# Kernel tuning notes

Measured on AMD Instinct MI355X. Metric: run time of the kernel, lower is better.

The kernel has to match this reference:

```python
import jax, jax.numpy as jnp
import numpy as np

N, E, B, D = 50000, 1600000, 256, 64


def _lin(k, fan_in, fan_out):
    kw, kb = jax.random.split(k)
    bound = 1.0 / np.sqrt(fan_in)
    w = jax.random.uniform(kw, (fan_in, fan_out), jnp.float32, -bound, bound)
    b = jax.random.uniform(kb, (fan_out,), jnp.float32, -bound, bound)
    return w, b


def setup_inputs() -> dict:
    key = jax.random.key(0)
    ks = jax.random.split(key, 16)
    inp = {
        "x": jax.random.normal(ks[0], (N, D), jnp.float32),
        "edge_attr": jax.random.normal(ks[1], (E, D), jnp.float32),
        "u": jax.random.normal(ks[2], (B, D), jnp.float32),
        "edge_index": jax.random.randint(ks[3], (2, E), 0, N, jnp.int32),
        "batch": jnp.sort(jax.random.randint(ks[4], (N,), 0, B, jnp.int32)),
    }
    # three MLPs: edge (in 4D), node (in 3D), global (in 3D); dims [2D, 2D, D]
    specs = [("e", 4 * D), ("n", 3 * D), ("g", 3 * D)]
    ki = 5
    for name, in_dim in specs:
        dims = [in_dim, 2 * D, 2 * D, D]
        for li in range(3):
            w, b = _lin(ks[ki], dims[li], dims[li + 1]); ki += 1
            inp[f"{name}w{li+1}"] = w
            inp[f"{name}b{li+1}"] = b
    return inp


def _mlp(h, w1, b1, w2, b2, w3, b3):
    h = h @ w1 + b1
    h = jax.nn.relu(h) @ w2 + b2
    h = jax.nn.relu(h) @ w3 + b3
    return h


def _scatter_mean(src, idx, num_segments):
    s = jax.ops.segment_sum(src, idx, num_segments=num_segments)
    c = jax.ops.segment_sum(jnp.ones_like(src[:, :1]), idx, num_segments=num_segments)
    return s / jnp.maximum(c, 1.0)


def reference(x, edge_attr, u,
              ew1, eb1, ew2, eb2, ew3, eb3,
              nw1, nb1, nw2, nb2, nw3, nb3,
              gw1, gb1, gw2, gb2, gw3, gb3,
              edge_index, batch):
    row, col = edge_index[0], edge_index[1]
    # edge model: cat[src, dest, edge_attr, u[batch[row]]] -> MLP
    e_in = jnp.concatenate([x[row], x[col], edge_attr, u[batch[row]]], axis=1)  # [E, 4D]
    e = _mlp(e_in, ew1, eb1, ew2, eb2, ew3, eb3)  # [E, D]
    # node model: scatter_mean(edge_attr', row) cat x cat u[batch] -> MLP
    n_agg = _scatter_mean(e, row, x.shape[0])  # [N, D]
    n_in = jnp.concatenate([n_agg, x, u[batch]], axis=1)  # [N, 3D]
    xn = _mlp(n_in, nw1, nb1, nw2, nb2, nw3, nb3)  # [N, D]
    # global model: cat[u, scatter_mean(x', batch), scatter_mean(e', batch[row])]
    edge_mean = _scatter_mean(e, batch[row], u.shape[0])  # [B, D]
    node_mean = _scatter_mean(xn, batch, u.shape[0])  # [B, D]
    g_in = jnp.concatenate([u, node_mean, edge_mean], axis=1)  # [B, 3D]
    un = _mlp(g_in, gw1, gb1, gw2, gb2, gw3, gb3)  # [B, D]
    return xn, e, un
```

## Files before the change

### kernel.cpp

```cpp
#include <hip/hip_runtime.h>

#define NN 50000
#define EE 1600000
#define BBATCH 256
#define DD 64

typedef _Float16 f16;
typedef _Float16 f16x8 __attribute__((ext_vector_type(8)));
typedef float f32x4 __attribute__((ext_vector_type(4)));

#define MFMA16(a,b,c) __builtin_amdgcn_mfma_f32_16x16x32_f16((a),(b),(c),0,0,0)

constexpr int EW1_RL  = 264;
constexpr int EW1_OFF = 0;
constexpr int EW2_OFF = EW1_OFF + 128 * EW1_RL;
constexpr int EW3_OFF = EW2_OFF + 128 * 136;
constexpr int EH_OFF  = EW3_OFF + 64 * 136;
constexpr int EB_OFF  = EH_OFF + 4 * 32 * 136;
constexpr int ELDS    = EB_OFF + 640;

constexpr int NW1_RL  = 200;
constexpr int NW1_OFF = 0;
constexpr int NW2_OFF = NW1_OFF + 128 * NW1_RL;
constexpr int NW3_OFF = NW2_OFF + 128 * 136;
constexpr int NH_OFF  = NW3_OFF + 64 * 136;
constexpr int NB_OFF  = NH_OFF + 4 * 32 * 136;
constexpr int NLDS    = NB_OFF + 640;

__device__ __forceinline__ f16x8 pack8(const float* __restrict__ p) {
  f32x4 a = *(const f32x4*)p;
  f32x4 b = *(const f32x4*)(p + 4);
  f16x8 r;
  r[0]=(f16)a[0]; r[1]=(f16)a[1]; r[2]=(f16)a[2]; r[3]=(f16)a[3];
  r[4]=(f16)b[0]; r[5]=(f16)b[1]; r[6]=(f16)b[2]; r[7]=(f16)b[3];
  return r;
}
__device__ __forceinline__ f16x8 pack8s(const float* __restrict__ p, float sc) {
  f32x4 a = *(const f32x4*)p;
  f32x4 b = *(const f32x4*)(p + 4);
  a = a * sc; b = b * sc;
  f16x8 r;
  r[0]=(f16)a[0]; r[1]=(f16)a[1]; r[2]=(f16)a[2]; r[3]=(f16)a[3];
  r[4]=(f16)b[0]; r[5]=(f16)b[1]; r[6]=(f16)b[2]; r[7]=(f16)b[3];
  return r;
}
__device__ __forceinline__ f16x8 cvt8(f32x4 a, f32x4 b) {
  f16x8 r;
  r[0]=(f16)a[0]; r[1]=(f16)a[1]; r[2]=(f16)a[2]; r[3]=(f16)a[3];
  r[4]=(f16)b[0]; r[5]=(f16)b[1]; r[6]=(f16)b[2]; r[7]=(f16)b[3];
  return r;
}

template<int KSL, int W1RL, int W1O, int W2O, int W3O>
__device__ __forceinline__ void mlp3_core(f16* __restrict__ sm,
    const float* __restrict__ b1l, const float* __restrict__ b2l,
    const float* __restrict__ b3l,
    const f16x8 (&A1)[2][KSL], const int hb, const int r15, const int g,
    f32x4 (&acc3)[2][4])
{
  #pragma unroll
  for (int hh = 0; hh < 2; ++hh) {
    f32x4 acc[2][4];
    #pragma unroll
    for (int nt = 0; nt < 4; ++nt) {
      const float bv = b1l[(hh*4 + nt)*16 + r15];
      acc[0][nt] = (f32x4){bv, bv, bv, bv};
      acc[1][nt] = acc[0][nt];
    }
    #pragma unroll
    for (int s = 0; s < KSL; ++s) {
      #pragma unroll
      for (int nt = 0; nt < 4; ++nt) {
        const f16x8 bf = *(const f16x8*)&sm[W1O + ((hh*4+nt)*16 + r15) * W1RL + s*32 + g*8];
        acc[0][nt] = MFMA16(A1[0][s], bf, acc[0][nt]);
        acc[1][nt] = MFMA16(A1[1][s], bf, acc[1][nt]);
      }
    }
    #pragma unroll
    for (int mt = 0; mt < 2; ++mt)
      #pragma unroll
      for (int nt = 0; nt < 4; ++nt)
        #pragma unroll
        for (int i = 0; i < 4; ++i)
          sm[hb + (mt*16 + g*4 + i)*136 + (hh*4+nt)*16 + r15] =
              (f16)fmaxf(acc[mt][nt][i], 0.f);
  }

  f16x8 A2[2][4];
  #pragma unroll
  for (int mt = 0; mt < 2; ++mt)
    #pragma unroll
    for (int s = 0; s < 4; ++s)
      A2[mt][s] = *(const f16x8*)&sm[hb + (mt*16 + r15)*136 + s*32 + g*8];

  #pragma unroll
  for (int hh = 0; hh < 2; ++hh) {
    f32x4 acc[2][4];
    #pragma unroll
    for (int nt = 0; nt < 4; ++nt) {
      const float bv = b2l[(hh*4 + nt)*16 + r15];
      acc[0][nt] = (f32x4){bv, bv, bv, bv};
      acc[1][nt] = acc[0][nt];
    }
    #pragma unroll
    for (int s = 0; s < 4; ++s) {
      #pragma unroll
      for (int nt = 0; nt < 4; ++nt) {
        const f16x8 bf = *(const f16x8*)&sm[W2O + ((hh*4+nt)*16 + r15)*136 + s*32 + g*8];
        acc[0][nt] = MFMA16(A2[0][s], bf, acc[0][nt]);
        acc[1][nt] = MFMA16(A2[1][s], bf, acc[1][nt]);
      }
    }
    #pragma unroll
    for (int mt = 0; mt < 2; ++mt)
      #pragma unroll
      for (int nt = 0; nt < 4; ++nt)
        #pragma unroll
        for (int i = 0; i < 4; ++i)
          sm[hb + (mt*16 + g*4 + i)*136 + (hh*4+nt)*16 + r15] =
              (f16)fmaxf(acc[mt][nt][i], 0.f);
  }

  f16x8 A3[2][4];
  #pragma unroll
  for (int mt = 0; mt < 2; ++mt)
    #pragma unroll
    for (int s = 0; s < 4; ++s)
      A3[mt][s] = *(const f16x8*)&sm[hb + (mt*16 + r15)*136 + s*32 + g*8];

  #pragma unroll
  for (int nt = 0; nt < 4; ++nt) {
    const float bv = b3l[nt*16 + r15];
    acc3[0][nt] = (f32x4){bv, bv, bv, bv};
    acc3[1][nt] = acc3[0][nt];
  }
  #pragma unroll
  for (int s = 0; s < 4; ++s) {
    #pragma unroll
    for (int nt = 0; nt < 4; ++nt) {
      const f16x8 bf = *(const f16x8*)&sm[W3O + (nt*16 + r15)*136 + s*32 + g*8];
      acc3[0][nt] = MFMA16(A3[0][s], bf, acc3[0][nt]);
      acc3[1][nt] = MFMA16(A3[1][s], bf, acc3[1][nt]);
    }
  }
}

__global__ void transpose_cvt(const float* __restrict__ w, f16* __restrict__ wt,
                              int in_dim, int out_dim) {
  int tid = blockIdx.x * 256 + threadIdx.x;
  int total = in_dim * out_dim;
  if (tid < total) {
    int o = tid / in_dim, i = tid - o * in_dim;
    wt[tid] = (f16)w[(size_t)i * out_dim + o];
  }
}

__global__ void count_kernel(const int* __restrict__ ei, int* __restrict__ deg) {
  int tid = blockIdx.x * 256 + threadIdx.x;
  if (tid < EE) atomicAdd(&deg[ei[tid]], 1);
}

__global__ __launch_bounds__(1024) void scan_kernel(const int* __restrict__ deg,
                                                    int* __restrict__ offs,
                                                    int* __restrict__ cursor) {
  const int t = threadIdx.x;
  const int per = (NN + 1023) / 1024;
  const int s0 = t * per;
  int s1 = s0 + per; if (s1 > NN) s1 = NN;
  int sum = 0;
  for (int i = s0; i < s1; ++i) sum += deg[i];
  const int lane = t & 63, wid = t >> 6;
  int v = sum;
  #pragma unroll
  for (int off = 1; off < 64; off <<= 1) {
    int o = __shfl_up(v, off);
    if (lane >= off) v += o;
  }
  __shared__ int wsums[16];
  __shared__ int wexcl[16];
  if (lane == 63) wsums[wid] = v;
  __syncthreads();
  if (t == 0) { int run = 0; for (int k = 0; k < 16; ++k) { wexcl[k] = run; run += wsums[k]; } }
  __syncthreads();
  int run = wexcl[wid] + v - sum;
  for (int i = s0; i < s1; ++i) { int d = deg[i]; offs[i] = run; cursor[i] = run; run += d; }
  if (t == 1023) offs[NN] = run;
}

__global__ void fill_kernel(const int* __restrict__ ei, int* __restrict__ cursor,
                            int* __restrict__ elist) {
  int tid = blockIdx.x * 256 + threadIdx.x;
  if (tid < EE) {
    int r = ei[tid];
    int pos = atomicAdd(&cursor[r], 1);
    elist[pos] = tid;
  }
}

__global__ __launch_bounds__(256, 1) void edge_mlp_kernel(
    const float* __restrict__ x, const float* __restrict__ ea,
    const float* __restrict__ u, const int* __restrict__ ei,
    const int* __restrict__ batch,
    const f16* __restrict__ w1t, const f16* __restrict__ w2t, const f16* __restrict__ w3t,
    const float* __restrict__ b1, const float* __restrict__ b2, const float* __restrict__ b3,
    float* __restrict__ e_out)
{
  __shared__ __align__(16) f16 sm[ELDS];
  const int t = threadIdx.x;
  for (int c = t; c < 4096; c += 256) { int r = c >> 5, kc = c & 31;
    *(uint4*)&sm[EW1_OFF + r*EW1_RL + kc*8] = *(const uint4*)&w1t[r*256 + kc*8]; }
  for (int c = t; c < 2048; c += 256) { int r = c >> 4, kc = c & 15;
    *(uint4*)&sm[EW2_OFF + r*136 + kc*8] = *(const uint4*)&w2t[r*128 + kc*8]; }
  for (int c = t; c < 1024; c += 256) { int r = c >> 4, kc = c & 15;
    *(uint4*)&sm[EW3_OFF + r*136 + kc*8] = *(const uint4*)&w3t[r*128 + kc*8]; }
  float* bias = (float*)&sm[EB_OFF];
  if (t < 128) { bias[t] = b1[t]; bias[128 + t] = b2[t]; }
  if (t < 64)  { bias[256 + t] = b3[t]; }
  __syncthreads();

  const int l = t & 63, w = t >> 6;
  const int r15 = l & 15, g = l >> 4;
  const int hb = EH_OFF + w * (32 * 136);
  const float* b1l = bias;
  const float* b2l = bias + 128;
  const float* b3l = bias + 256;

  const int stride = gridDim.x;
  const int t0 = blockIdx.x;
  const int NT = EE / 128;

  int rC[2], cC[2], bC[2];
  int rN[2], cN[2], bN[2];
  f32x4 G[2][8][2];
  f16x8 A1[2][8];

  auto issueG = [&](const int (&rr)[2], const int (&cc)[2], const int (&bb)[2], int tt) {
    #pragma unroll
    for (int mt = 0; mt < 2; ++mt) {
      const float* s0p = x  + (size_t)rr[mt] * 64 + g * 8;
      const float* s1p = x  + (size_t)cc[mt] * 64 + g * 8;
      const float* s2p = ea + ((size_t)(tt * 128 + w * 32 + mt * 16 + r15)) * 64 + g * 8;
      const float* s3p = u  + (size_t)bb[mt] * 64 + g * 8;
      #pragma unroll
      for (int s = 0; s < 8; ++s) {
        const float* p = (s < 2 ? s0p : s < 4 ? s1p : s < 6 ? s2p : s3p) + (s & 1) * 32;
        G[mt][s][0] = *(const f32x4*)p;
        G[mt][s][1] = *(const f32x4*)(p + 4);
      }
    }
  };

  {
    int rr[2], cc[2], bb[2];
    #pragma unroll
    for (int mt = 0; mt < 2; ++mt) {
      const int eid = t0 * 128 + w * 32 + mt * 16 + r15;
      rr[mt] = ei[eid]; cc[mt] = ei[EE + eid];
    }
    #pragma unroll
    for (int mt = 0; mt < 2; ++mt) bb[mt] = batch[rr[mt]];
    issueG(rr, cc, bb, t0);
    int t1 = t0 + stride; if (t1 >= NT) t1 = t0;
    #pragma unroll
    for (int mt = 0; mt < 2; ++mt) {
      const int eid = t1 * 128 + w * 32 + mt * 16 + r15;
      rC[mt] = ei[eid]; cC[mt] = ei[EE + eid];
    }
    #pragma unroll
    for (int mt = 0; mt < 2; ++mt) bC[mt] = batch[rC[mt]];
  }

  for (int tile = t0; tile < NT; tile += stride) {
    #pragma unroll
    for (int mt = 0; mt < 2; ++mt)
      #pragma unroll
      for (int s = 0; s < 8; ++s)
        A1[mt][s] = cvt8(G[mt][s][0], G[mt][s][1]);

    int t2 = tile + 2 * stride; if (t2 >= NT) t2 = t0;
    #pragma unroll
    for (int mt = 0; mt < 2; ++mt) {
      const int eid = t2 * 128 + w * 32 + mt * 16 + r15;
      rN[mt] = ei[eid]; cN[mt] = ei[EE + eid];
    }
    int t1 = tile + stride; if (t1 >= NT) t1 = t0;
    issueG(rC, cC, bC, t1);

    f32x4 acc3[2][4];
    mlp3_core<8, EW1_RL, EW1_OFF, EW2_OFF, EW3_OFF>(sm, b1l, b2l, b3l, A1, hb, r15, g, acc3);

    #pragma unroll
    for (int mt = 0; mt < 2; ++mt) bN[mt] = batch[rN[mt]];

    const int base = tile * 128 + w * 32;
    #pragma unroll
    for (int mt = 0; mt < 2; ++mt)
      #pragma unroll
      for (int nt = 0; nt < 4; ++nt)
        #pragma unroll
        for (int i = 0; i < 4; ++i) {
          const int m = base + mt * 16 + g * 4 + i;
          e_out[(size_t)m * 64 + nt * 16 + r15] = acc3[mt][nt][i];
        }

    #pragma unroll
    for (int mt = 0; mt < 2; ++mt) { rC[mt] = rN[mt]; cC[mt] = cN[mt]; bC[mt] = bN[mt]; }
  }
}

__global__ void nsum_kernel(const float* __restrict__ e_src, const int* __restrict__ offs,
                            const int* __restrict__ elist, float* __restrict__ n_sum) {
  const int l = threadIdx.x & 63;
  const int wid = (blockIdx.x * blockDim.x + threadIdx.x) >> 6;
  const int nw = (gridDim.x * blockDim.x) >> 6;
  for (int node = wid; node < NN; node += nw) {
    const int s = offs[node], e = offs[node + 1];
    float acc = 0.f;
    int j = s;
    for (; j + 4 <= e; j += 4) {
      const int e0 = elist[j], e1 = elist[j+1], e2 = elist[j+2], e3 = elist[j+3];
      float v0 = e_src[(size_t)e0 * 64 + l];
      float v1 = e_src[(size_t)e1 * 64 + l];
      float v2 = e_src[(size_t)e2 * 64 + l];
      float v3 = e_src[(size_t)e3 * 64 + l];
      acc += (v0 + v1) + (v2 + v3);
    }
    for (; j < e; ++j) acc += e_src[(size_t)elist[j] * 64 + l];
    n_sum[(size_t)node * 64 + l] = acc;
  }
}

__global__ __launch_bounds__(256, 1) void node_mlp_kernel(
    const float* __restrict__ x, const float* __restrict__ u,
    const int* __restrict__ batch, const float* __restrict__ n_sum,
    const int* __restrict__ deg,
    const f16* __restrict__ w1t, const f16* __restrict__ w2t, const f16* __restrict__ w3t,
    const float* __restrict__ b1, const float* __restrict__ b2, const float* __restrict__ b3,
    float* __restrict__ xn_out)
{
  __shared__ __align__(16) f16 sm[NLDS];
  const int t = threadIdx.x;
  for (int c = t; c < 3072; c += 256) { int r = c / 24, kc = c - r * 24;
    *(uint4*)&sm[NW1_OFF + r*NW1_RL + kc*8] = *(const uint4*)&w1t[r*192 + kc*8]; }
  for (int c = t; c < 2048; c += 256) { int r = c >> 4, kc = c & 15;
    *(uint4*)&sm[NW2_OFF + r*136 + kc*8] = *(const uint4*)&w2t[r*128 + kc*8]; }
  for (int c = t; c < 1024; c += 256) { int r = c >> 4, kc = c & 15;
    *(uint4*)&sm[NW3_OFF + r*136 + kc*8] = *(const uint4*)&w3t[r*128 + kc*8]; }
  float* bias = (float*)&sm[NB_OFF];
  if (t < 128) { bias[t] = b1[t]; bias[128 + t] = b2[t]; }
  if (t < 64)  { bias[256 + t] = b3[t]; }
  __syncthreads();

  const int l = t & 63, w = t >> 6;
  const int r15 = l & 15, g = l >> 4;
  const int hb = NH_OFF + w * (32 * 136);
  const int base = blockIdx.x * 128 + w * 32;

  f16x8 A1[2][6];
  #pragma unroll
  for (int mt = 0; mt < 2; ++mt) {
    int raw = base + mt * 16 + r15;
    int node = raw < NN ? raw : NN - 1;
    float inv = 1.0f / fmaxf((float)deg[node], 1.0f);
    const float* sA = n_sum + (size_t)node * 64;
    const float* sB = x + (size_t)node * 64;
    const float* sC = u + (size_t)batch[node] * 64;
    #pragma unroll
    for (int s = 0; s < 6; ++s) {
      const int off = (s & 1) * 32 + g * 8;
      if (s < 2)      A1[mt][s] = pack8s(sA + off, inv);
      else if (s < 4) A1[mt][s] = pack8(sB + off);
      else            A1[mt][s] = pack8(sC + off);
    }
  }
  f32x4 acc3[2][4];
  mlp3_core<6, NW1_RL, NW1_OFF, NW2_OFF, NW3_OFF>(sm, bias, bias + 128, bias + 256,
                                                  A1, hb, r15, g, acc3);
  #pragma unroll
  for (int mt = 0; mt < 2; ++mt)
    #pragma unroll
    for (int nt = 0; nt < 4; ++nt)
      #pragma unroll
      for (int i = 0; i < 4; ++i) {
        const int m = base + mt * 16 + g * 4 + i;
        if (m < NN) xn_out[(size_t)m * 64 + nt * 16 + r15] = acc3[mt][nt][i];
      }
}

__global__ void bstart_kernel(const int* __restrict__ batch, int* __restrict__ bstart) {
  int tid = blockIdx.x * 256 + threadIdx.x;
  if (tid >= NN) return;
  int b = batch[tid];
  if (tid == 0) { for (int k = 0; k <= b; ++k) bstart[k] = 0; }
  else { int pb = batch[tid - 1]; for (int k = pb + 1; k <= b; ++k) bstart[k] = tid; }
  if (tid == NN - 1) { for (int k = b + 1; k <= BBATCH; ++k) bstart[k] = NN; }
}

__global__ void batch_sum_kernel(const float* __restrict__ xn, const float* __restrict__ n_sum,
                                 const int* __restrict__ deg, const int* __restrict__ bstart,
                                 float* __restrict__ nbsum, float* __restrict__ ebsum,
                                 int* __restrict__ ncnt, int* __restrict__ ecnt) {
  __shared__ float red0[256];
  __shared__ float red1[256];
  __shared__ int   redi[256];
  const int b = blockIdx.x;
  const int s = bstart[b], e = bstart[b + 1];
  const int t = threadIdx.x, c = t & 63, j0 = t >> 6;
  float xs = 0.f, ns = 0.f; int dc = 0;
  for (int j = s + j0; j < e; j += 4) {
    xs += xn[(size_t)j * 64 + c];
    ns += n_sum[(size_t)j * 64 + c];
    if (c == 0) dc += deg[j];
  }
  red0[t] = xs; red1[t] = ns; redi[t] = dc;
  __syncthreads();
  if (t < 128) { red0[t] += red0[t + 128]; red1[t] += red1[t + 128]; redi[t] += redi[t + 128]; }
  __syncthreads();
  if (t < 64) {
    float a0 = red0[t] + red0[t + 64];
    float a1 = red1[t] + red1[t + 64];
    nbsum[b * 64 + t] = a0;
    ebsum[b * 64 + t] = a1;
    if (t == 0) { ncnt[b] = e - s; ecnt[b] = redi[0] + redi[64]; }
  }
}

__global__ __launch_bounds__(256, 1) void global_mlp_kernel(
    const float* __restrict__ u, const float* __restrict__ nbsum,
    const float* __restrict__ ebsum, const int* __restrict__ ncnt,
    const int* __restrict__ ecnt,
    const f16* __restrict__ w1t, const f16* __restrict__ w2t, const f16* __restrict__ w3t,
    const float* __restrict__ b1, const float* __restrict__ b2, const float* __restrict__ b3,
    float* __restrict__ un_out)
{
  __shared__ __align__(16) f16 sm[NLDS];
  const int t = threadIdx.x;
  for (int c = t; c < 3072; c += 256) { int r = c / 24, kc = c - r * 24;
    *(uint4*)&sm[NW1_OFF + r*NW1_RL + kc*8] = *(const uint4*)&w1t[r*192 + kc*8]; }
  for (int c = t; c < 2048; c += 256) { int r = c >> 4, kc = c & 15;
    *(uint4*)&sm[NW2_OFF + r*136 + kc*8] = *(const uint4*)&w2t[r*128 + kc*8]; }
  for (int c = t; c < 1024; c += 256) { int r = c >> 4, kc = c & 15;
    *(uint4*)&sm[NW3_OFF + r*136 + kc*8] = *(const uint4*)&w3t[r*128 + kc*8]; }
  float* bias = (float*)&sm[NB_OFF];
  if (t < 128) { bias[t] = b1[t]; bias[128 + t] = b2[t]; }
  if (t < 64)  { bias[256 + t] = b3[t]; }
  __syncthreads();

  const int l = t & 63, w = t >> 6;
  const int r15 = l & 15, g = l >> 4;
  const int hb = NH_OFF + w * (32 * 136);
  const int base = blockIdx.x * 128 + w * 32;

  f16x8 A1[2][6];
  #pragma unroll
  for (int mt = 0; mt < 2; ++mt) {
    const int r = base + mt * 16 + r15;
    const float invn = 1.0f / fmaxf((float)ncnt[r], 1.0f);
    const float inve = 1.0f / fmaxf((float)ecnt[r], 1.0f);
    const float* sA = u + (size_t)r * 64;
    const float* sB = nbsum + (size_t)r * 64;
    const float* sC = ebsum + (size_t)r * 64;
    #pragma unroll
    for (int s = 0; s < 6; ++s) {
      const int off = (s & 1) * 32 + g * 8;
      if (s < 2)      A1[mt][s] = pack8(sA + off);
      else if (s < 4) A1[mt][s] = pack8s(sB + off, invn);
      else            A1[mt][s] = pack8s(sC + off, inve);
    }
  }
  f32x4 acc3[2][4];
  mlp3_core<6, NW1_RL, NW1_OFF, NW2_OFF, NW3_OFF>(sm, bias, bias + 128, bias + 256,
                                                  A1, hb, r15, g, acc3);
  #pragma unroll
  for (int mt = 0; mt < 2; ++mt)
    #pragma unroll
    for (int nt = 0; nt < 4; ++nt)
      #pragma unroll
      for (int i = 0; i < 4; ++i) {
        const int m = base + mt * 16 + g * 4 + i;
        un_out[(size_t)m * 64 + nt * 16 + r15] = acc3[mt][nt][i];
      }
}

extern "C" void kernel_launch(void* const* d_in, const int* in_sizes, int n_in,
                              void* d_out, int out_size, void* d_ws, size_t ws_size,
                              hipStream_t stream)
{
  (void)in_sizes; (void)n_in; (void)out_size; (void)ws_size;
  const float* x     = (const float*)d_in[0];
  const float* ea    = (const float*)d_in[1];
  const float* u     = (const float*)d_in[2];
  const int*   ei    = (const int*)d_in[3];
  const int*   batch = (const int*)d_in[4];
  const float* ew1 = (const float*)d_in[5];  const float* eb1 = (const float*)d_in[6];
  const float* ew2 = (const float*)d_in[7];  const float* eb2 = (const float*)d_in[8];
  const float* ew3 = (const float*)d_in[9];  const float* eb3 = (const float*)d_in[10];
  const float* nw1 = (const float*)d_in[11]; const float* nb1 = (const float*)d_in[12];
  const float* nw2 = (const float*)d_in[13]; const float* nb2 = (const float*)d_in[14];
  const float* nw3 = (const float*)d_in[15]; const float* nb3 = (const float*)d_in[16];
  const float* gw1 = (const float*)d_in[17]; const float* gb1 = (const float*)d_in[18];
  const float* gw2 = (const float*)d_in[19]; const float* gb2 = (const float*)d_in[20];
  const float* gw3 = (const float*)d_in[21]; const float* gb3 = (const float*)d_in[22];

  float* xn_out = (float*)d_out;
  float* e_out  = xn_out + (size_t)NN * DD;
  float* un_out = e_out + (size_t)EE * DD;

  char* p = (char*)d_ws;
  auto alloc = [&](size_t bytes) -> void* {
    void* r = (void*)p; p += (bytes + 255) & ~(size_t)255; return r;
  };
  f16* wtE1 = (f16*)alloc(256 * 128 * 2);
  f16* wtE2 = (f16*)alloc(128 * 128 * 2);
  f16* wtE3 = (f16*)alloc(128 * 64 * 2);
  f16* wtN1 = (f16*)alloc(192 * 128 * 2);
  f16* wtN2 = (f16*)alloc(128 * 128 * 2);
  f16* wtN3 = (f16*)alloc(128 * 64 * 2);
  f16* wtG1 = (f16*)alloc(192 * 128 * 2);
  f16* wtG2 = (f16*)alloc(128 * 128 * 2);
  f16* wtG3 = (f16*)alloc(128 * 64 * 2);
  int* deg    = (int*)alloc((size_t)NN * 4);
  int* offs   = (int*)alloc((size_t)(NN + 1) * 4);
  int* cursor = (int*)alloc((size_t)NN * 4);
  int* elist  = (int*)alloc((size_t)EE * 4);
  int* bstart = (int*)alloc((size_t)(BBATCH + 1) * 4);
  float* nbsum = (float*)alloc((size_t)BBATCH * 64 * 4);
  float* ebsum = (float*)alloc((size_t)BBATCH * 64 * 4);
  int* ncnt = (int*)alloc((size_t)BBATCH * 4);
  int* ecnt = (int*)alloc((size_t)BBATCH * 4);
  float* n_sum = (float*)alloc((size_t)NN * 64 * 4);

  transpose_cvt<<<dim3((256*128 + 255)/256), dim3(256), 0, stream>>>(ew1, wtE1, 256, 128);
  transpose_cvt<<<dim3((128*128 + 255)/256), dim3(256), 0, stream>>>(ew2, wtE2, 128, 128);
  transpose_cvt<<<dim3((128*64  + 255)/256), dim3(256), 0, stream>>>(ew3, wtE3, 128, 64);
  transpose_cvt<<<dim3((192*128 + 255)/256), dim3(256), 0, stream>>>(nw1, wtN1, 192, 128);
  transpose_cvt<<<dim3((128*128 + 255)/256), dim3(256), 0, stream>>>(nw2, wtN2, 128, 128);
  transpose_cvt<<<dim3((128*64  + 255)/256), dim3(256), 0, stream>>>(nw3, wtN3, 128, 64);
  transpose_cvt<<<dim3((192*128 + 255)/256), dim3(256), 0, stream>>>(gw1, wtG1, 192, 128);
  transpose_cvt<<<dim3((128*128 + 255)/256), dim3(256), 0, stream>>>(gw2, wtG2, 128, 128);
  transpose_cvt<<<dim3((128*64  + 255)/256), dim3(256), 0, stream>>>(gw3, wtG3, 128, 64);

  hipMemsetAsync(deg, 0, (size_t)NN * 4, stream);
  count_kernel<<<dim3(6250), dim3(256), 0, stream>>>(ei, deg);
  scan_kernel<<<dim3(1), dim3(1024), 0, stream>>>(deg, offs, cursor);
  fill_kernel<<<dim3(6250), dim3(256), 0, stream>>>(ei, cursor, elist);

  edge_mlp_kernel<<<dim3(256), dim3(256), 0, stream>>>(
      x, ea, u, ei, batch, wtE1, wtE2, wtE3, eb1, eb2, eb3, e_out);

  nsum_kernel<<<dim3(2048), dim3(256), 0, stream>>>(e_out, offs, elist, n_sum);

  node_mlp_kernel<<<dim3((NN + 127) / 128), dim3(256), 0, stream>>>(
      x, u, batch, n_sum, deg, wtN1, wtN2, wtN3, nb1, nb2, nb3, xn_out);

  bstart_kernel<<<dim3((NN + 255) / 256), dim3(256), 0, stream>>>(batch, bstart);
  batch_sum_kernel<<<dim3(BBATCH), dim3(256), 0, stream>>>(
      xn_out, n_sum, deg, bstart, nbsum, ebsum, ncnt, ecnt);

  global_mlp_kernel<<<dim3(2), dim3(256), 0, stream>>>(
      u, nbsum, ebsum, ncnt, ecnt, wtG1, wtG2, wtG3, gb1, gb2, gb3, un_out);
}
```

Before: 842.7 us.

## Widen edge MLP blocks, inline MLP with overlapped gathers, add fp16 edge copy for aggregation

```diff
diff --git a/kernel.cpp b/kernel.cpp
--- a/kernel.cpp
+++ b/kernel.cpp
@@ -16,7 +16,7 @@
 constexpr int EW2_OFF = EW1_OFF + 128 * EW1_RL;
 constexpr int EW3_OFF = EW2_OFF + 128 * 136;
 constexpr int EH_OFF  = EW3_OFF + 64 * 136;
-constexpr int EB_OFF  = EH_OFF + 4 * 32 * 136;
+constexpr int EB_OFF  = EH_OFF + 8 * 16 * 136;
 constexpr int ELDS    = EB_OFF + 640;
 
 constexpr int NW1_RL  = 200;
@@ -145,14 +145,26 @@
   }
 }
 
-__global__ void transpose_cvt(const float* __restrict__ w, f16* __restrict__ wt,
-                              int in_dim, int out_dim) {
+__global__ void transpose_all(
+    const float* __restrict__ e1, const float* __restrict__ e2, const float* __restrict__ e3,
+    const float* __restrict__ n1, const float* __restrict__ n2, const float* __restrict__ n3,
+    const float* __restrict__ q1, const float* __restrict__ q2, const float* __restrict__ q3,
+    f16* __restrict__ dst) {
   int tid = blockIdx.x * 256 + threadIdx.x;
-  int total = in_dim * out_dim;
-  if (tid < total) {
-    int o = tid / in_dim, i = tid - o * in_dim;
-    wt[tid] = (f16)w[(size_t)i * out_dim + o];
-  }
+  const int o1=32768,o2=49152,o3=57344,o4=81920,o5=98304,o6=106496,o7=131072,o8=147456,o9=155648;
+  if (tid >= o9) return;
+  const float* src; int in, od, rel;
+  if      (tid < o1) { src=e1; in=256; od=128; rel=tid;    }
+  else if (tid < o2) { src=e2; in=128; od=128; rel=tid-o1; }
+  else if (tid < o3) { src=e3; in=128; od=64;  rel=tid-o2; }
+  else if (tid < o4) { src=n1; in=192; od=128; rel=tid-o3; }
+  else if (tid < o5) { src=n2; in=128; od=128; rel=tid-o4; }
+  else if (tid < o6) { src=n3; in=128; od=64;  rel=tid-o5; }
+  else if (tid < o7) { src=q1; in=192; od=128; rel=tid-o6; }
+  else if (tid < o8) { src=q2; in=128; od=128; rel=tid-o7; }
+  else               { src=q3; in=128; od=64;  rel=tid-o8; }
+  int o = rel / in, i = rel - o * in;
+  dst[tid] = (f16)src[(size_t)i * od + o];
 }
 
 __global__ void count_kernel(const int* __restrict__ ei, int* __restrict__ deg) {
@@ -197,37 +209,33 @@
   }
 }
 
-__global__ __launch_bounds__(256, 1) void edge_mlp_kernel(
+__global__ __launch_bounds__(512, 2) void edge_mlp_kernel(
     const float* __restrict__ x, const float* __restrict__ ea,
     const float* __restrict__ u, const int* __restrict__ ei,
     const int* __restrict__ batch,
     const f16* __restrict__ w1t, const f16* __restrict__ w2t, const f16* __restrict__ w3t,
     const float* __restrict__ b1, const float* __restrict__ b2, const float* __restrict__ b3,
-    float* __restrict__ e_out)
+    float* __restrict__ e_out, f16* __restrict__ e16)
 {
   __shared__ __align__(16) f16 sm[ELDS];
   const int t = threadIdx.x;
-  for (int c = t; c < 4096; c += 256) { int r = c >> 5, kc = c & 31;
+  for (int c = t; c < 4096; c += 512) { int r = c >> 5, kc = c & 31;
     *(uint4*)&sm[EW1_OFF + r*EW1_RL + kc*8] = *(const uint4*)&w1t[r*256 + kc*8]; }
-  for (int c = t; c < 2048; c += 256) { int r = c >> 4, kc = c & 15;
+  for (int c = t; c < 2048; c += 512) { int r = c >> 4, kc = c & 15;
     *(uint4*)&sm[EW2_OFF + r*136 + kc*8] = *(const uint4*)&w2t[r*128 + kc*8]; }
-  for (int c = t; c < 1024; c += 256) { int r = c >> 4, kc = c & 15;
+  for (int c = t; c < 1024; c += 512) { int r = c >> 4, kc = c & 15;
     *(uint4*)&sm[EW3_OFF + r*136 + kc*8] = *(const uint4*)&w3t[r*128 + kc*8]; }
   float* bias = (float*)&sm[EB_OFF];
   if (t < 128) { bias[t] = b1[t]; bias[128 + t] = b2[t]; }
-  if (t < 64)  { bias[256 + t] = b3[t]; }
+  else if (t < 192) { bias[256 + (t - 128)] = b3[t - 128]; }
   __syncthreads();
 
   const int l = t & 63, w = t >> 6;
   const int r15 = l & 15, g = l >> 4;
-  const int hb = EH_OFF + w * (32 * 136);
-  const float* b1l = bias;
-  const float* b2l = bias + 128;
-  const float* b3l = bias + 256;
-
+  const int hb = EH_OFF + w * (16 * 136);
+  const int NT = EE / 256;
   const int stride = gridDim.x;
   const int t0 = blockIdx.x;
-  const int NT = EE / 128;
 
   int rC[2], cC[2], bC[2];
   int rN[2], cN[2], bN[2];
@@ -239,7 +247,7 @@
     for (int mt = 0; mt < 2; ++mt) {
       const float* s0p = x  + (size_t)rr[mt] * 64 + g * 8;
       const float* s1p = x  + (size_t)cc[mt] * 64 + g * 8;
-      const float* s2p = ea + ((size_t)(tt * 128 + w * 32 + mt * 16 + r15)) * 64 + g * 8;
+      const float* s2p = ea + ((size_t)(tt * 256 + w * 32 + mt * 16 + r15)) * 64 + g * 8;
       const float* s3p = u  + (size_t)bb[mt] * 64 + g * 8;
       #pragma unroll
       for (int s = 0; s < 8; ++s) {
@@ -254,7 +262,7 @@
     int rr[2], cc[2], bb[2];
     #pragma unroll
     for (int mt = 0; mt < 2; ++mt) {
-      const int eid = t0 * 128 + w * 32 + mt * 16 + r15;
+      const int eid = t0 * 256 + w * 32 + mt * 16 + r15;
       rr[mt] = ei[eid]; cc[mt] = ei[EE + eid];
     }
     #pragma unroll
@@ -263,36 +271,127 @@
     int t1 = t0 + stride; if (t1 >= NT) t1 = t0;
     #pragma unroll
     for (int mt = 0; mt < 2; ++mt) {
-      const int eid = t1 * 128 + w * 32 + mt * 16 + r15;
+      const int eid = t1 * 256 + w * 32 + mt * 16 + r15;
       rC[mt] = ei[eid]; cC[mt] = ei[EE + eid];
     }
     #pragma unroll
     for (int mt = 0; mt < 2; ++mt) bC[mt] = batch[rC[mt]];
-  }
-
-  for (int tile = t0; tile < NT; tile += stride) {
     #pragma unroll
     for (int mt = 0; mt < 2; ++mt)
       #pragma unroll
       for (int s = 0; s < 8; ++s)
         A1[mt][s] = cvt8(G[mt][s][0], G[mt][s][1]);
-
+  }
+
+  for (int tile = t0; tile < NT; tile += stride) {
     int t2 = tile + 2 * stride; if (t2 >= NT) t2 = t0;
     #pragma unroll
     for (int mt = 0; mt < 2; ++mt) {
-      const int eid = t2 * 128 + w * 32 + mt * 16 + r15;
+      const int eid = t2 * 256 + w * 32 + mt * 16 + r15;
       rN[mt] = ei[eid]; cN[mt] = ei[EE + eid];
     }
+
+    f32x4 acc1[2][2][4];
+    #pragma unroll
+    for (int hh = 0; hh < 2; ++hh)
+      #pragma unroll
+      for (int nt = 0; nt < 4; ++nt) {
+        const float bv = bias[hh*64 + nt*16 + r15];
+        acc1[hh][0][nt] = (f32x4){bv, bv, bv, bv};
+        acc1[hh][1][nt] = acc1[hh][0][nt];
+      }
+    #pragma unroll
+    for (int s = 0; s < 8; ++s)
+      #pragma unroll
+      for (int hh = 0; hh < 2; ++hh)
+        #pragma unroll
+        for (int nt = 0; nt < 4; ++nt) {
+          const f16x8 bf = *(const f16x8*)&sm[EW1_OFF + (hh*64 + nt*16 + r15)*EW1_RL + s*32 + g*8];
+          acc1[hh][0][nt] = MFMA16(A1[0][s], bf, acc1[hh][0][nt]);
+          acc1[hh][1][nt] = MFMA16(A1[1][s], bf, acc1[hh][1][nt]);
+        }
+
+    #pragma unroll
+    for (int mt = 0; mt < 2; ++mt) bN[mt] = batch[rN[mt]];
+
+    f16x8 A2[2][4];
+    #pragma unroll
+    for (int mt = 0; mt < 2; ++mt) {
+      #pragma unroll
+      for (int hh = 0; hh < 2; ++hh)
+        #pragma unroll
+        for (int nt = 0; nt < 4; ++nt)
+          #pragma unroll
+          for (int i = 0; i < 4; ++i)
+            sm[hb + (g*4 + i)*136 + hh*64 + nt*16 + r15] =
+                (f16)fmaxf(acc1[hh][mt][nt][i], 0.f);
+      #pragma unroll
+      for (int s = 0; s < 4; ++s)
+        A2[mt][s] = *(const f16x8*)&sm[hb + r15*136 + s*32 + g*8];
+    }
+
     int t1 = tile + stride; if (t1 >= NT) t1 = t0;
     issueG(rC, cC, bC, t1);
 
+    f32x4 acc2[2][2][4];
+    #pragma unroll
+    for (int hh = 0; hh < 2; ++hh)
+      #pragma unroll
+      for (int nt = 0; nt < 4; ++nt) {
+        const float bv = bias[128 + hh*64 + nt*16 + r15];
+        acc2[hh][0][nt] = (f32x4){bv, bv, bv, bv};
+        acc2[hh][1][nt] = acc2[hh][0][nt];
+      }
+    #pragma unroll
+    for (int s = 0; s < 4; ++s)
+      #pragma unroll
+      for (int hh = 0; hh < 2; ++hh)
+        #pragma unroll
+        for (int nt = 0; nt < 4; ++nt) {
+          const f16x8 bf = *(const f16x8*)&sm[EW2_OFF + (hh*64 + nt*16 + r15)*136 + s*32 + g*8];
+          acc2[hh][0][nt] = MFMA16(A2[0][s], bf, acc2[hh][0][nt]);
+          acc2[hh][1][nt] = MFMA16(A2[1][s], bf, acc2[hh][1][nt]);
+        }
+
+    f16x8 A3[2][4];
+    #pragma unroll
+    for (int mt = 0; mt < 2; ++mt) {
+      #pragma unroll
+      for (int hh = 0; hh < 2; ++hh)
+        #pragma unroll
+        for (int nt = 0; nt < 4; ++nt)
+          #pragma unroll
+          for (int i = 0; i < 4; ++i)
+            sm[hb + (g*4 + i)*136 + hh*64 + nt*16 + r15] =
+                (f16)fmaxf(acc2[hh][mt][nt][i], 0.f);
+      #pragma unroll
+      for (int s = 0; s < 4; ++s)
+        A3[mt][s] = *(const f16x8*)&sm[hb + r15*136 + s*32 + g*8];
+    }
+
+    #pragma unroll
+    for (int mt = 0; mt < 2; ++mt)
+      #pragma unroll
+      for (int s = 0; s < 8; ++s)
+        A1[mt][s] = cvt8(G[mt][s][0], G[mt][s][1]);
+
     f32x4 acc3[2][4];
-    mlp3_core<8, EW1_RL, EW1_OFF, EW2_OFF, EW3_OFF>(sm, b1l, b2l, b3l, A1, hb, r15, g, acc3);
-
-    #pragma unroll
-    for (int mt = 0; mt < 2; ++mt) bN[mt] = batch[rN[mt]];
-
-    const int base = tile * 128 + w * 32;
+    #pragma unroll
+    for (int nt = 0; nt < 4; ++nt) {
+      const float bv = bias[256 + nt*16 + r15];
+      acc3[0][nt] = (f32x4){bv, bv, bv, bv};
+      acc3[1][nt] = acc3[0][nt];
+    }
+    #pragma unroll
+    for (int s = 0; s < 4; ++s)
+      #pragma unroll
+      for (int nt = 0; nt < 4; ++nt) {
+        const f16x8 bf = *(const f16x8*)&sm[EW3_OFF + (nt*16 + r15)*136 + s*32 + g*8];
+        acc3[0][nt] = MFMA16(A3[0][s], bf, acc3[0][nt]);
+        acc3[1][nt] = MFMA16(A3[1][s], bf, acc3[1][nt]);
+      }
+
+    const int base = tile * 256 + w * 32;
     #pragma unroll
     for (int mt = 0; mt < 2; ++mt)
       #pragma unroll
@@ -300,7 +399,9 @@
         #pragma unroll
         for (int i = 0; i < 4; ++i) {
           const int m = base + mt * 16 + g * 4 + i;
-          e_out[(size_t)m * 64 + nt * 16 + r15] = acc3[mt][nt][i];
+          const float v = acc3[mt][nt][i];
+          e_out[(size_t)m * 64 + nt * 16 + r15] = v;
+          if (e16) e16[(size_t)m * 64 + nt * 16 + r15] = (f16)v;
         }
 
     #pragma unroll
@@ -308,7 +409,8 @@
   }
 }
 
-__global__ void nsum_kernel(const float* __restrict__ e_src, const int* __restrict__ offs,
+__global__ void nsum_kernel(const float* __restrict__ e_src, const f16* __restrict__ e16,
+                            const int* __restrict__ offs,
                             const int* __restrict__ elist, float* __restrict__ n_sum) {
   const int l = threadIdx.x & 63;
   const int wid = (blockIdx.x * blockDim.x + threadIdx.x) >> 6;
@@ -317,15 +419,27 @@
     const int s = offs[node], e = offs[node + 1];
     float acc = 0.f;
     int j = s;
-    for (; j + 4 <= e; j += 4) {
-      const int e0 = elist[j], e1 = elist[j+1], e2 = elist[j+2], e3 = elist[j+3];
-      float v0 = e_src[(size_t)e0 * 64 + l];
-      float v1 = e_src[(size_t)e1 * 64 + l];
-      float v2 = e_src[(size_t)e2 * 64 + l];
-      float v3 = e_src[(size_t)e3 * 64 + l];
-      acc += (v0 + v1) + (v2 + v3);
-    }
-    for (; j < e; ++j) acc += e_src[(size_t)elist[j] * 64 + l];
+    if (e16) {
+      for (; j + 4 <= e; j += 4) {
+        const int e0 = elist[j], e1 = elist[j+1], e2 = elist[j+2], e3 = elist[j+3];
+        float v0 = (float)e16[(size_t)e0 * 64 + l];
+        float v1 = (float)e16[(size_t)e1 * 64 + l];
+        float v2 = (float)e16[(size_t)e2 * 64 + l];
+        float v3 = (float)e16[(size_t)e3 * 64 + l];
+        acc += (v0 + v1) + (v2 + v3);
+      }
+      for (; j < e; ++j) acc += (float)e16[(size_t)elist[j] * 64 + l];
+    } else {
+      for (; j + 4 <= e; j += 4) {
+        const int e0 = elist[j], e1 = elist[j+1], e2 = elist[j+2], e3 = elist[j+3];
+        float v0 = e_src[(size_t)e0 * 64 + l];
+        float v1 = e_src[(size_t)e1 * 64 + l];
+        float v2 = e_src[(size_t)e2 * 64 + l];
+        float v3 = e_src[(size_t)e3 * 64 + l];
+        acc += (v0 + v1) + (v2 + v3);
+      }
+      for (; j < e; ++j) acc += e_src[(size_t)elist[j] * 64 + l];
+    }
     n_sum[(size_t)node * 64 + l] = acc;
   }
 }
@@ -486,7 +600,7 @@
                               void* d_out, int out_size, void* d_ws, size_t ws_size,
                               hipStream_t stream)
 {
-  (void)in_sizes; (void)n_in; (void)out_size; (void)ws_size;
+  (void)in_sizes; (void)n_in; (void)out_size;
   const float* x     = (const float*)d_in[0];
   const float* ea    = (const float*)d_in[1];
   const float* u     = (const float*)d_in[2];
@@ -529,26 +643,25 @@
   int* ncnt = (int*)alloc((size_t)BBATCH * 4);
   int* ecnt = (int*)alloc((size_t)BBATCH * 4);
   float* n_sum = (float*)alloc((size_t)NN * 64 * 4);
-
-  transpose_cvt<<<dim3((256*128 + 255)/256), dim3(256), 0, stream>>>(ew1, wtE1, 256, 128);
-  transpose_cvt<<<dim3((128*128 + 255)/256), dim3(256), 0, stream>>>(ew2, wtE2, 128, 128);
-  transpose_cvt<<<dim3((128*64  + 255)/256), dim3(256), 0, stream>>>(ew3, wtE3, 128, 64);
-  transpose_cvt<<<dim3((192*128 + 255)/256), dim3(256), 0, stream>>>(nw1, wtN1, 192, 128);
-  transpose_cvt<<<dim3((128*128 + 255)/256), dim3(256), 0, stream>>>(nw2, wtN2, 128, 128);
-  transpose_cvt<<<dim3((128*64  + 255)/256), dim3(256), 0, stream>>>(nw3, wtN3, 128, 64);
-  transpose_cvt<<<dim3((192*128 + 255)/256), dim3(256), 0, stream>>>(gw1, wtG1, 192, 128);
-  transpose_cvt<<<dim3((128*128 + 255)/256), dim3(256), 0, stream>>>(gw2, wtG2, 128, 128);
-  transpose_cvt<<<dim3((128*64  + 255)/256), dim3(256), 0, stream>>>(gw3, wtG3, 128, 64);
+  f16* e16 = nullptr;
+  {
+    size_t used = (size_t)(p - (char*)d_ws);
+    size_t need = (size_t)EE * 64 * 2;
+    if (ws_size >= used + need) e16 = (f16*)alloc(need);
+  }
+
+  transpose_all<<<dim3(608), dim3(256), 0, stream>>>(
+      ew1, ew2, ew3, nw1, nw2, nw3, gw1, gw2, gw3, wtE1);
 
   hipMemsetAsync(deg, 0, (size_t)NN * 4, stream);
   count_kernel<<<dim3(6250), dim3(256), 0, stream>>>(ei, deg);
   scan_kernel<<<dim3(1), dim3(1024), 0, stream>>>(deg, offs, cursor);
   fill_kernel<<<dim3(6250), dim3(256), 0, stream>>>(ei, cursor, elist);
 
-  edge_mlp_kernel<<<dim3(256), dim3(256), 0, stream>>>(
-      x, ea, u, ei, batch, wtE1, wtE2, wtE3, eb1, eb2, eb3, e_out);
-
-  nsum_kernel<<<dim3(2048), dim3(256), 0, stream>>>(e_out, offs, elist, n_sum);
+  edge_mlp_kernel<<<dim3(256), dim3(512), 0, stream>>>(
+      x, ea, u, ei, batch, wtE1, wtE2, wtE3, eb1, eb2, eb3, e_out, e16);
+
+  nsum_kernel<<<dim3(2048), dim3(256), 0, stream>>>(e_out, e16, offs, elist, n_sum);
 
   node_mlp_kernel<<<dim3((NN + 127) / 128), dim3(256), 0, stream>>>(
       x, u, batch, n_sum, deg, wtN1, wtN2, wtN3, nb1, nb2, nb3, xn_out);
```

After: 935.3 us. +11.0%, slower.
